# Kernel tuning notes

Hardware: AMD Instinct MI355X
Metric: run time of the kernel (lower is better)

Reference implementation:

```python
import jax, jax.numpy as jnp
import numpy as np
import math

NB_STEPS = 32  # quadrature steps (nb_steps init arg)
HID = 256      # num_hiddens init arg


def _cc_quadrature(nb):
    """Clenshaw-Curtis weights/nodes exactly as in the UMNN reference code."""
    k = np.arange(nb + 1)
    lam = np.cos(np.outer(k, k) * math.pi / nb)
    lam[:, 0] = 0.5
    lam[:, -1] *= 0.5
    lam = lam * 2.0 / nb
    W = k.astype(np.float64).copy()
    W[1::2] = 0.0
    Wv = 2.0 / (1.0 - W ** 2)
    Wv[0] = 1.0
    Wv[1::2] = 0.0
    cc_w = lam.T @ Wv                      # (nb+1,)
    steps = np.cos(k * math.pi / nb)       # (nb+1,) in [-1, 1]
    return cc_w.astype(np.float32), steps.astype(np.float32)

CC_W, CC_STEPS = _cc_quadrature(NB_STEPS)


def setup_inputs() -> dict:
    key = jax.random.key(0)
    ks = jax.random.split(key, 8)
    logits = jax.random.normal(ks[0], (1024, 10), jnp.float32)

    def lin_init(k, shape, fan_in):
        b = 1.0 / np.sqrt(fan_in)
        return jax.random.uniform(k, shape, jnp.float32, -b, b)

    return {
        "logits": logits,
        "W1": lin_init(ks[1], (1, HID), 1),
        "b1": lin_init(ks[2], (HID,), 1),
        "W2": lin_init(ks[3], (HID, HID), HID),
        "b2": lin_init(ks[4], (HID,), HID),
        "W3": lin_init(ks[5], (HID, 1), HID),
        "b3": lin_init(ks[6], (1,), HID),
        "offset": jnp.zeros((1,), jnp.float32),
    }


def _integrand(t, W1, b1, W2, b2, W3, b3):
    # t: (N, S) scalar evaluation points -> strictly positive integrand (N, S)
    h = jax.nn.elu(t[..., None] * W1[0] + b1)                 # (N, S, HID)
    h = jax.nn.elu(jnp.einsum('nsh,hk->nsk', h, W2) + b2)     # (N, S, HID)
    o = jnp.einsum('nsh,ho->nso', h, W3)[..., 0] + b3[0]      # (N, S)
    return jax.nn.elu(o) + 1.0


def reference(logits, W1, b1, W2, b2, W3, b3, offset):
    # 1) log-softmax normalization
    z = logits - jax.nn.logsumexp(logits, axis=1, keepdims=True)
    # 2) standardize with frozen buffers meanlogit=0, logitstd=1 (identity here)
    # 3) flatten and apply monotonic NN: F(x) = offset + int_0^x g(t) dt
    x = z.reshape(-1)                                         # (N,)
    steps = jnp.asarray(CC_STEPS)                             # (S,)
    ccw = jnp.asarray(CC_W)                                   # (S,)
    t = x[:, None] * (steps + 1.0) * 0.5                      # (N, S) nodes in [0, x]
    g = _integrand(t, W1, b1, W2, b2, W3, b3)                 # (N, S)
    integral = (g @ ccw) * (x * 0.5)                          # (N,)
    return (integral + offset[0]).reshape(logits.shape)
```

## Files before the change

kernel.cpp:

```cpp
#include <hip/hip_runtime.h>

typedef _Float16 f16x8 __attribute__((ext_vector_type(8)));
typedef float floatx4 __attribute__((ext_vector_type(4)));

#define NPTS   10240
#define GRID   2112
#define GM1    2111.0f
#define NBLK_MLP 22

#define WS_STEPS 0
#define WS_CCW   256
#define WS_MINX  512
#define WS_X     1024
#define WS_W2IMG 65536
#define WS_G     196608

__device__ __forceinline__ float elu1(float v) {
  return v > 0.f ? v : __expf(v) - 1.f;
}

__device__ __forceinline__ void gload_lds16(const void* g, void* l) {
  __builtin_amdgcn_global_load_lds(
      (const __attribute__((address_space(1))) unsigned int*)g,
      (__attribute__((address_space(3))) unsigned int*)l,
      16, 0, 0);
}

__global__ void k_pre(const float* __restrict__ logits,
                      const float* __restrict__ W2,
                      unsigned char* __restrict__ ws)
{
  __shared__ float red[256];
  const int bid = blockIdx.x, tid = threadIdx.x;
  if (bid < 32) {
    int u    = (bid << 8) + tid;
    int col  = u & 127;
    int rest = u >> 7;
    int k16l = rest & 15;
    int q    = rest >> 4;
    int c    = q >> 1, kh = q & 1;
    int kbase = kh * 128 + k16l * 8;
    int j     = c * 128 + col;
    union { _Float16 h[8]; uint4 v; } pk;
    #pragma unroll
    for (int i = 0; i < 8; ++i)
      pk.h[i] = (_Float16)W2[(kbase + i) * 256 + j];
    unsigned off = (unsigned)q * 32768u + (unsigned)col * 256u
                 + (unsigned)((k16l ^ (col & 7)) << 4);
    *(uint4*)(ws + WS_W2IMG + off) = pk.v;
  } else if (bid == 32) {
    if (tid <= 32) {
      const double pi = 3.141592653589793238462643383279502884;
      float* steps = (float*)(ws + WS_STEPS);
      float* ccw   = (float*)(ws + WS_CCW);
      steps[tid] = (float)cos((double)tid * pi / 32.0);
      double acc = 0.0;
      for (int i = 0; i <= 32; i += 2) {
        double wv = (i == 0) ? 1.0 : 2.0 / (1.0 - (double)(i * i));
        double L  = cos((double)(i * tid) * pi / 32.0);
        if (tid == 0)  L = 0.5;
        if (tid == 32) L *= 0.5;
        acc += L * wv;
      }
      ccw[tid] = (float)(acc * (1.0 / 16.0));
    }
  } else {
    int r = ((bid - 33) << 8) + tid;
    const float* row = logits + r * 10;
    float* x = (float*)(ws + WS_X);
    float v[10]; float m = -3.0e38f;
    #pragma unroll
    for (int c = 0; c < 10; ++c) { v[c] = row[c]; m = fmaxf(m, v[c]); }
    float s = 0.f;
    #pragma unroll
    for (int c = 0; c < 10; ++c) s += __expf(v[c] - m);
    float lse = m + __logf(s);
    float lmin = 3.0e38f;
    #pragma unroll
    for (int c = 0; c < 10; ++c) {
      float z = v[c] - lse;
      x[r * 10 + c] = z;
      lmin = fminf(lmin, z);
    }
    red[tid] = lmin;
    __syncthreads();
    #pragma unroll
    for (int t = 128; t > 0; t >>= 1) {
      if (tid < t) red[tid] = fminf(red[tid], red[tid + t]);
      __syncthreads();
    }
    if (tid == 0)
      atomicMax((unsigned*)(ws + WS_MINX), __float_as_uint(red[0]));
  }
}

__global__ __launch_bounds__(256, 2) void k_mlp(
    const unsigned char* __restrict__ ws,
    const float* __restrict__ W1, const float* __restrict__ b1,
    const float* __restrict__ b2, const float* __restrict__ W3,
    const float* __restrict__ b3)
{
  __shared__ unsigned char smem[65536] __attribute__((aligned(16)));
  const int tid  = threadIdx.x;
  const int lane = tid & 63, wid = tid >> 6;
  const int wm = wid >> 1, wn = wid & 1;
  const int l15 = lane & 15, l4 = lane >> 4;

  const unsigned char* img = ws + WS_W2IMG;
  float* g_out = (float*)(const_cast<unsigned char*>(ws) + WS_G);
  const float minx   = __uint_as_float(*(const unsigned*)(ws + WS_MINX));
  const float step_t = minx * (-1.0f / GM1);

  const int row_base = blockIdx.x * 96;

  #pragma unroll
  for (int i = 0; i < 8; ++i) {
    int off = wid * 1024 + i * 4096;
    gload_lds16(img + off + lane * 16, smem + off);
  }

  float b2r[2][4], w3r[2][4];
  #pragma unroll
  for (int c = 0; c < 2; ++c)
    #pragma unroll
    for (int bj = 0; bj < 4; ++bj) {
      int col = c * 128 + wn * 64 + bj * 16 + l15;
      b2r[c][bj] = b2[col];
      w3r[c][bj] = W3[col];
    }

  f16x8 A[3][8];
  {
    float t[3];
    #pragma unroll
    for (int ai = 0; ai < 3; ++ai) {
      int rg = row_base + wm * 48 + ai * 16 + l15;
      t[ai] = fmaf((float)rg, step_t, minx);
    }
    #pragma unroll
    for (int ks = 0; ks < 8; ++ks) {
      int k0 = ks * 32 + l4 * 8;
      float w1v[8], b1v[8];
      *(float4*)&w1v[0] = *(const float4*)(W1 + k0);
      *(float4*)&w1v[4] = *(const float4*)(W1 + k0 + 4);
      *(float4*)&b1v[0] = *(const float4*)(b1 + k0);
      *(float4*)&b1v[4] = *(const float4*)(b1 + k0 + 4);
      #pragma unroll
      for (int ai = 0; ai < 3; ++ai) {
        union { _Float16 h[8]; f16x8 v; } pk;
        #pragma unroll
        for (int j = 0; j < 8; ++j)
          pk.h[j] = (_Float16)elu1(fmaf(t[ai], w1v[j], b1v[j]));
        A[ai][ks] = pk.v;
      }
    }
  }
  __syncthreads();

  float pacc[3][4];
  #pragma unroll
  for (int a = 0; a < 3; ++a)
    #pragma unroll
    for (int r = 0; r < 4; ++r) pacc[a][r] = 0.f;

  floatx4 acc[3][4];

  #pragma unroll
  for (int q = 0; q < 4; ++q) {
    const int buf = (q & 1) * 32768;
    if (q < 3) {
      const int nb = ((q + 1) & 1) * 32768;
      #pragma unroll
      for (int i = 0; i < 8; ++i) {
        int off = wid * 1024 + i * 4096;
        gload_lds16(img + (q + 1) * 32768 + off + lane * 16, smem + nb + off);
      }
    }
    if ((q & 1) == 0) {
      #pragma unroll
      for (int a = 0; a < 3; ++a)
        #pragma unroll
        for (int bj = 0; bj < 4; ++bj) acc[a][bj] = floatx4{0.f, 0.f, 0.f, 0.f};
    }
    const int kh = q & 1;
    #pragma unroll
    for (int kl = 0; kl < 4; ++kl) {
      const int ks = kh * 4 + kl;
      f16x8 bfr[4];
      #pragma unroll
      for (int bj = 0; bj < 4; ++bj) {
        int col  = wn * 64 + bj * 16 + l15;
        int unit = (kl * 4 + l4) ^ (col & 7);
        bfr[bj]  = *(const f16x8*)(smem + buf + col * 256 + (unit << 4));
      }
      #pragma unroll
      for (int ai = 0; ai < 3; ++ai)
        #pragma unroll
        for (int bj = 0; bj < 4; ++bj)
          acc[ai][bj] = __builtin_amdgcn_mfma_f32_16x16x32_f16(
              A[ai][ks], bfr[bj], acc[ai][bj], 0, 0, 0);
    }
    if (q & 1) {
      const int c = q >> 1;
      #pragma unroll
      for (int bj = 0; bj < 4; ++bj) {
        float b2v = b2r[c][bj], w3v = w3r[c][bj];
        #pragma unroll
        for (int ai = 0; ai < 3; ++ai)
          #pragma unroll
          for (int rr = 0; rr < 4; ++rr)
            pacc[ai][rr] = fmaf(elu1(acc[ai][bj][rr] + b2v), w3v, pacc[ai][rr]);
      }
    }
    __syncthreads();
  }

  float* part = (float*)smem;
  #pragma unroll
  for (int ai = 0; ai < 3; ++ai)
    #pragma unroll
    for (int rr = 0; rr < 4; ++rr) {
      float v = pacc[ai][rr];
      v += __shfl_xor(v, 1);
      v += __shfl_xor(v, 2);
      v += __shfl_xor(v, 4);
      v += __shfl_xor(v, 8);
      if (l15 == 0) part[wid * 48 + ai * 16 + l4 * 4 + rr] = v;
    }
  __syncthreads();
  if (tid < 96) {
    int wmr = tid / 48, r = tid - wmr * 48;
    float o = part[(wmr * 2) * 48 + r] + part[(wmr * 2 + 1) * 48 + r] + b3[0];
    g_out[row_base + wmr * 48 + r] = elu1(o) + 1.f;
  }
}

__global__ void k_interp(const unsigned char* __restrict__ ws,
                         const float* __restrict__ offset,
                         float* __restrict__ out)
{
  __shared__ float gs[GRID];
  __shared__ float st_l[33], cw_l[33];
  const int tid = threadIdx.x;
  const float* gg = (const float*)(ws + WS_G);
  #pragma unroll
  for (int i = tid; i < GRID; i += 256) gs[i] = gg[i];
  if (tid < 33) {
    st_l[tid] = ((const float*)(ws + WS_STEPS))[tid];
    cw_l[tid] = ((const float*)(ws + WS_CCW))[tid];
  }
  __syncthreads();

  const int n = blockIdx.x * 256 + tid;
  const float x    = ((const float*)(ws + WS_X))[n];
  const float minx = __uint_as_float(*(const unsigned*)(ws + WS_MINX));
  const float xo   = x / minx;
  const float a    = xo * (0.5f * GM1);
  const float c0   = GM1 - a;
  float acc = 0.f;
  #pragma unroll 4
  for (int s = 0; s < 33; ++s) {
    float u = fmaf(-a, st_l[s], c0);
    int i = (int)u;
    i = i > (GRID - 2) ? (GRID - 2) : i;
    i = i < 0 ? 0 : i;
    float f  = u - (float)i;
    float g0 = gs[i], g1 = gs[i + 1];
    acc = fmaf(cw_l[s], fmaf(f, g1 - g0, g0), acc);
  }
  out[n] = fmaf(acc, x * 0.5f, offset[0]);
}

extern "C" void kernel_launch(void* const* d_in, const int* in_sizes, int n_in,
                              void* d_out, int out_size, void* d_ws, size_t ws_size,
                              hipStream_t stream)
{
  const float* logits = (const float*)d_in[0];
  const float* W1     = (const float*)d_in[1];
  const float* b1     = (const float*)d_in[2];
  const float* W2     = (const float*)d_in[3];
  const float* b2     = (const float*)d_in[4];
  const float* W3     = (const float*)d_in[5];
  const float* b3     = (const float*)d_in[6];
  const float* offset = (const float*)d_in[7];
  unsigned char* ws   = (unsigned char*)d_ws;
  float* out          = (float*)d_out;

  k_pre<<<37, 256, 0, stream>>>(logits, W2, ws);
  k_mlp<<<NBLK_MLP, 256, 0, stream>>>(ws, W1, b1, b2, W3, b3);
  k_interp<<<40, 256, 0, stream>>>(ws, offset, out);
}
```

Measured before the change: 86.98 us.

## Fuse three kernels into one cooperative kernel with grid-wide syncs

Merges the preprocessing, MLP, and interpolation kernels into a single cooperative launch of 40 blocks, with grid.sync barriers between the phases. The Clenshaw-Curtis nodes and weights are now computed per block in fast float cosine instead of in double precision by a dedicated block. The aim is to remove two kernel launch gaps and the related dependency overhead. The costs are grid-sync latency, a cooperative launch, and slightly lower precision in the quadrature constants.

```diff
diff --git a/kernel.cpp b/kernel.cpp
--- a/kernel.cpp
+++ b/kernel.cpp
@@ -1,15 +1,16 @@
 #include <hip/hip_runtime.h>
+#include <hip/hip_cooperative_groups.h>
+
+namespace cg = cooperative_groups;
 
 typedef _Float16 f16x8 __attribute__((ext_vector_type(8)));
 typedef float floatx4 __attribute__((ext_vector_type(4)));
 
-#define NPTS   10240
-#define GRID   2112
-#define GM1    2111.0f
+#define GRID_T   2112
+#define GM1      2111.0f
 #define NBLK_MLP 22
-
-#define WS_STEPS 0
-#define WS_CCW   256
+#define NBLOCKS  40
+
 #define WS_MINX  512
 #define WS_X     1024
 #define WS_W2IMG 65536
@@ -26,12 +27,18 @@
       16, 0, 0);
 }
 
-__global__ void k_pre(const float* __restrict__ logits,
-                      const float* __restrict__ W2,
-                      unsigned char* __restrict__ ws)
+__global__ __launch_bounds__(256, 2) void k_fused(
+    const float* __restrict__ logits,
+    const float* __restrict__ W1, const float* __restrict__ b1,
+    const float* __restrict__ W2, const float* __restrict__ b2,
+    const float* __restrict__ W3, const float* __restrict__ b3,
+    const float* __restrict__ offset,
+    unsigned char* __restrict__ ws, float* __restrict__ out)
 {
-  __shared__ float red[256];
+  __shared__ unsigned char smem[65536] __attribute__((aligned(16)));
+  cg::grid_group grid = cg::this_grid();
   const int bid = blockIdx.x, tid = threadIdx.x;
+
   if (bid < 32) {
     int u    = (bid << 8) + tid;
     int col  = u & 127;
@@ -48,24 +55,9 @@
     unsigned off = (unsigned)q * 32768u + (unsigned)col * 256u
                  + (unsigned)((k16l ^ (col & 7)) << 4);
     *(uint4*)(ws + WS_W2IMG + off) = pk.v;
-  } else if (bid == 32) {
-    if (tid <= 32) {
-      const double pi = 3.141592653589793238462643383279502884;
-      float* steps = (float*)(ws + WS_STEPS);
-      float* ccw   = (float*)(ws + WS_CCW);
-      steps[tid] = (float)cos((double)tid * pi / 32.0);
-      double acc = 0.0;
-      for (int i = 0; i <= 32; i += 2) {
-        double wv = (i == 0) ? 1.0 : 2.0 / (1.0 - (double)(i * i));
-        double L  = cos((double)(i * tid) * pi / 32.0);
-        if (tid == 0)  L = 0.5;
-        if (tid == 32) L *= 0.5;
-        acc += L * wv;
-      }
-      ccw[tid] = (float)(acc * (1.0 / 16.0));
-    }
-  } else {
-    int r = ((bid - 33) << 8) + tid;
+  } else if (bid < 36) {
+    float* red = (float*)smem;
+    int r = ((bid - 32) << 8) + tid;
     const float* row = logits + r * 10;
     float* x = (float*)(ws + WS_X);
     float v[10]; float m = -3.0e38f;
@@ -92,183 +84,185 @@
     if (tid == 0)
       atomicMax((unsigned*)(ws + WS_MINX), __float_as_uint(red[0]));
   }
-}
-
-__global__ __launch_bounds__(256, 2) void k_mlp(
-    const unsigned char* __restrict__ ws,
-    const float* __restrict__ W1, const float* __restrict__ b1,
-    const float* __restrict__ b2, const float* __restrict__ W3,
-    const float* __restrict__ b3)
-{
-  __shared__ unsigned char smem[65536] __attribute__((aligned(16)));
-  const int tid  = threadIdx.x;
-  const int lane = tid & 63, wid = tid >> 6;
-  const int wm = wid >> 1, wn = wid & 1;
-  const int l15 = lane & 15, l4 = lane >> 4;
-
-  const unsigned char* img = ws + WS_W2IMG;
-  float* g_out = (float*)(const_cast<unsigned char*>(ws) + WS_G);
-  const float minx   = __uint_as_float(*(const unsigned*)(ws + WS_MINX));
-  const float step_t = minx * (-1.0f / GM1);
-
-  const int row_base = blockIdx.x * 96;
-
-  #pragma unroll
-  for (int i = 0; i < 8; ++i) {
-    int off = wid * 1024 + i * 4096;
-    gload_lds16(img + off + lane * 16, smem + off);
+  grid.sync();
+
+  if (bid < NBLK_MLP) {
+    const int lane = tid & 63, wid = tid >> 6;
+    const int wm = wid >> 1, wn = wid & 1;
+    const int l15 = lane & 15, l4 = lane >> 4;
+
+    const unsigned char* img = ws + WS_W2IMG;
+    float* g_out = (float*)(ws + WS_G);
+    const float minx   = __uint_as_float(*(const unsigned*)(ws + WS_MINX));
+    const float step_t = minx * (-1.0f / GM1);
+
+    const int row_base = bid * 96;
+
+    #pragma unroll
+    for (int i = 0; i < 8; ++i) {
+      int off = wid * 1024 + i * 4096;
+      gload_lds16(img + off + lane * 16, smem + off);
+    }
+
+    float b2r[2][4], w3r[2][4];
+    #pragma unroll
+    for (int c = 0; c < 2; ++c)
+      #pragma unroll
+      for (int bj = 0; bj < 4; ++bj) {
+        int col = c * 128 + wn * 64 + bj * 16 + l15;
+        b2r[c][bj] = b2[col];
+        w3r[c][bj] = W3[col];
+      }
+
+    f16x8 A[3][8];
+    {
+      float t[3];
+      #pragma unroll
+      for (int ai = 0; ai < 3; ++ai) {
+        int rg = row_base + wm * 48 + ai * 16 + l15;
+        t[ai] = fmaf((float)rg, step_t, minx);
+      }
+      #pragma unroll
+      for (int ks = 0; ks < 8; ++ks) {
+        int k0 = ks * 32 + l4 * 8;
+        float w1v[8], b1v[8];
+        *(float4*)&w1v[0] = *(const float4*)(W1 + k0);
+        *(float4*)&w1v[4] = *(const float4*)(W1 + k0 + 4);
+        *(float4*)&b1v[0] = *(const float4*)(b1 + k0);
+        *(float4*)&b1v[4] = *(const float4*)(b1 + k0 + 4);
+        #pragma unroll
+        for (int ai = 0; ai < 3; ++ai) {
+          union { _Float16 h[8]; f16x8 v; } pk;
+          #pragma unroll
+          for (int j = 0; j < 8; ++j)
+            pk.h[j] = (_Float16)elu1(fmaf(t[ai], w1v[j], b1v[j]));
+          A[ai][ks] = pk.v;
+        }
+      }
+    }
+    __syncthreads();
+
+    float pacc[3][4];
+    #pragma unroll
+    for (int a = 0; a < 3; ++a)
+      #pragma unroll
+      for (int r = 0; r < 4; ++r) pacc[a][r] = 0.f;
+
+    floatx4 acc[3][4];
+
+    #pragma unroll
+    for (int q = 0; q < 4; ++q) {
+      const int buf = (q & 1) * 32768;
+      if (q < 3) {
+        const int nb = ((q + 1) & 1) * 32768;
+        #pragma unroll
+        for (int i = 0; i < 8; ++i) {
+          int off = wid * 1024 + i * 4096;
+          gload_lds16(img + (q + 1) * 32768 + off + lane * 16, smem + nb + off);
+        }
+      }
+      if ((q & 1) == 0) {
+        #pragma unroll
+        for (int a = 0; a < 3; ++a)
+          #pragma unroll
+          for (int bj = 0; bj < 4; ++bj) acc[a][bj] = floatx4{0.f, 0.f, 0.f, 0.f};
+      }
+      const int kh = q & 1;
+      #pragma unroll
+      for (int kl = 0; kl < 4; ++kl) {
+        const int ks = kh * 4 + kl;
+        f16x8 bfr[4];
+        #pragma unroll
+        for (int bj = 0; bj < 4; ++bj) {
+          int col  = wn * 64 + bj * 16 + l15;
+          int unit = (kl * 4 + l4) ^ (col & 7);
+          bfr[bj]  = *(const f16x8*)(smem + buf + col * 256 + (unit << 4));
+        }
+        #pragma unroll
+        for (int ai = 0; ai < 3; ++ai)
+          #pragma unroll
+          for (int bj = 0; bj < 4; ++bj)
+            acc[ai][bj] = __builtin_amdgcn_mfma_f32_16x16x32_f16(
+                A[ai][ks], bfr[bj], acc[ai][bj], 0, 0, 0);
+      }
+      if (q & 1) {
+        const int c = q >> 1;
+        #pragma unroll
+        for (int bj = 0; bj < 4; ++bj) {
+          float b2v = b2r[c][bj], w3v = w3r[c][bj];
+          #pragma unroll
+          for (int ai = 0; ai < 3; ++ai)
+            #pragma unroll
+            for (int rr = 0; rr < 4; ++rr)
+              pacc[ai][rr] = fmaf(elu1(acc[ai][bj][rr] + b2v), w3v, pacc[ai][rr]);
+        }
+      }
+      __syncthreads();
+    }
+
+    float* part = (float*)smem;
+    #pragma unroll
+    for (int ai = 0; ai < 3; ++ai)
+      #pragma unroll
+      for (int rr = 0; rr < 4; ++rr) {
+        float v = pacc[ai][rr];
+        v += __shfl_xor(v, 1);
+        v += __shfl_xor(v, 2);
+        v += __shfl_xor(v, 4);
+        v += __shfl_xor(v, 8);
+        if (l15 == 0) part[wid * 48 + ai * 16 + l4 * 4 + rr] = v;
+      }
+    __syncthreads();
+    if (tid < 96) {
+      int wmr = tid / 48, r = tid - wmr * 48;
+      float o = part[(wmr * 2) * 48 + r] + part[(wmr * 2 + 1) * 48 + r] + b3[0];
+      g_out[row_base + wmr * 48 + r] = elu1(o) + 1.f;
+    }
   }
-
-  float b2r[2][4], w3r[2][4];
-  #pragma unroll
-  for (int c = 0; c < 2; ++c)
-    #pragma unroll
-    for (int bj = 0; bj < 4; ++bj) {
-      int col = c * 128 + wn * 64 + bj * 16 + l15;
-      b2r[c][bj] = b2[col];
-      w3r[c][bj] = W3[col];
-    }
-
-  f16x8 A[3][8];
+  grid.sync();
+
   {
-    float t[3];
-    #pragma unroll
-    for (int ai = 0; ai < 3; ++ai) {
-      int rg = row_base + wm * 48 + ai * 16 + l15;
-      t[ai] = fmaf((float)rg, step_t, minx);
-    }
-    #pragma unroll
-    for (int ks = 0; ks < 8; ++ks) {
-      int k0 = ks * 32 + l4 * 8;
-      float w1v[8], b1v[8];
-      *(float4*)&w1v[0] = *(const float4*)(W1 + k0);
-      *(float4*)&w1v[4] = *(const float4*)(W1 + k0 + 4);
-      *(float4*)&b1v[0] = *(const float4*)(b1 + k0);
-      *(float4*)&b1v[4] = *(const float4*)(b1 + k0 + 4);
-      #pragma unroll
-      for (int ai = 0; ai < 3; ++ai) {
-        union { _Float16 h[8]; f16x8 v; } pk;
-        #pragma unroll
-        for (int j = 0; j < 8; ++j)
-          pk.h[j] = (_Float16)elu1(fmaf(t[ai], w1v[j], b1v[j]));
-        A[ai][ks] = pk.v;
-      }
-    }
+    float* gs   = (float*)smem;
+    float* st_l = (float*)(smem + GRID_T * 4);
+    float* cw_l = st_l + 33;
+    if (tid <= 32) {
+      const float pi32 = 3.14159265358979323846f / 32.f;
+      st_l[tid] = __cosf((float)tid * pi32);
+      float acc = 0.f;
+      #pragma unroll
+      for (int i = 0; i <= 32; i += 2) {
+        float wv = (i == 0) ? 1.f : 2.f / (1.f - (float)(i * i));
+        float L  = __cosf((float)((i * tid) & 63) * pi32);
+        if (tid == 0)  L = 0.5f;
+        if (tid == 32) L *= 0.5f;
+        acc += L * wv;
+      }
+      cw_l[tid] = acc * (1.0f / 16.0f);
+    }
+    const float* gg = (const float*)(ws + WS_G);
+    #pragma unroll
+    for (int i = tid; i < GRID_T; i += 256) gs[i] = gg[i];
+    __syncthreads();
+
+    const int n = bid * 256 + tid;
+    const float x    = ((const float*)(ws + WS_X))[n];
+    const float minx = __uint_as_float(*(const unsigned*)(ws + WS_MINX));
+    const float xo   = x / minx;
+    const float a    = xo * (0.5f * GM1);
+    const float c0   = GM1 - a;
+    float acc = 0.f;
+    #pragma unroll 4
+    for (int s = 0; s < 33; ++s) {
+      float u = fmaf(-a, st_l[s], c0);
+      int i = (int)u;
+      i = i > (GRID_T - 2) ? (GRID_T - 2) : i;
+      i = i < 0 ? 0 : i;
+      float f  = u - (float)i;
+      float g0 = gs[i], g1 = gs[i + 1];
+      acc = fmaf(cw_l[s], fmaf(f, g1 - g0, g0), acc);
+    }
+    out[n] = fmaf(acc, x * 0.5f, offset[0]);
   }
-  __syncthreads();
-
-  float pacc[3][4];
-  #pragma unroll
-  for (int a = 0; a < 3; ++a)
-    #pragma unroll
-    for (int r = 0; r < 4; ++r) pacc[a][r] = 0.f;
-
-  floatx4 acc[3][4];
-
-  #pragma unroll
-  for (int q = 0; q < 4; ++q) {
-    const int buf = (q & 1) * 32768;
-    if (q < 3) {
-      const int nb = ((q + 1) & 1) * 32768;
-      #pragma unroll
-      for (int i = 0; i < 8; ++i) {
-        int off = wid * 1024 + i * 4096;
-        gload_lds16(img + (q + 1) * 32768 + off + lane * 16, smem + nb + off);
-      }
-    }
-    if ((q & 1) == 0) {
-      #pragma unroll
-      for (int a = 0; a < 3; ++a)
-        #pragma unroll
-        for (int bj = 0; bj < 4; ++bj) acc[a][bj] = floatx4{0.f, 0.f, 0.f, 0.f};
-    }
-    const int kh = q & 1;
-    #pragma unroll
-    for (int kl = 0; kl < 4; ++kl) {
-      const int ks = kh * 4 + kl;
-      f16x8 bfr[4];
-      #pragma unroll
-      for (int bj = 0; bj < 4; ++bj) {
-        int col  = wn * 64 + bj * 16 + l15;
-        int unit = (kl * 4 + l4) ^ (col & 7);
-        bfr[bj]  = *(const f16x8*)(smem + buf + col * 256 + (unit << 4));
-      }
-      #pragma unroll
-      for (int ai = 0; ai < 3; ++ai)
-        #pragma unroll
-        for (int bj = 0; bj < 4; ++bj)
-          acc[ai][bj] = __builtin_amdgcn_mfma_f32_16x16x32_f16(
-              A[ai][ks], bfr[bj], acc[ai][bj], 0, 0, 0);
-    }
-    if (q & 1) {
-      const int c = q >> 1;
-      #pragma unroll
-      for (int bj = 0; bj < 4; ++bj) {
-        float b2v = b2r[c][bj], w3v = w3r[c][bj];
-        #pragma unroll
-        for (int ai = 0; ai < 3; ++ai)
-          #pragma unroll
-          for (int rr = 0; rr < 4; ++rr)
-            pacc[ai][rr] = fmaf(elu1(acc[ai][bj][rr] + b2v), w3v, pacc[ai][rr]);
-      }
-    }
-    __syncthreads();
-  }
-
-  float* part = (float*)smem;
-  #pragma unroll
-  for (int ai = 0; ai < 3; ++ai)
-    #pragma unroll
-    for (int rr = 0; rr < 4; ++rr) {
-      float v = pacc[ai][rr];
-      v += __shfl_xor(v, 1);
-      v += __shfl_xor(v, 2);
-      v += __shfl_xor(v, 4);
-      v += __shfl_xor(v, 8);
-      if (l15 == 0) part[wid * 48 + ai * 16 + l4 * 4 + rr] = v;
-    }
-  __syncthreads();
-  if (tid < 96) {
-    int wmr = tid / 48, r = tid - wmr * 48;
-    float o = part[(wmr * 2) * 48 + r] + part[(wmr * 2 + 1) * 48 + r] + b3[0];
-    g_out[row_base + wmr * 48 + r] = elu1(o) + 1.f;
-  }
-}
-
-__global__ void k_interp(const unsigned char* __restrict__ ws,
-                         const float* __restrict__ offset,
-                         float* __restrict__ out)
-{
-  __shared__ float gs[GRID];
-  __shared__ float st_l[33], cw_l[33];
-  const int tid = threadIdx.x;
-  const float* gg = (const float*)(ws + WS_G);
-  #pragma unroll
-  for (int i = tid; i < GRID; i += 256) gs[i] = gg[i];
-  if (tid < 33) {
-    st_l[tid] = ((const float*)(ws + WS_STEPS))[tid];
-    cw_l[tid] = ((const float*)(ws + WS_CCW))[tid];
-  }
-  __syncthreads();
-
-  const int n = blockIdx.x * 256 + tid;
-  const float x    = ((const float*)(ws + WS_X))[n];
-  const float minx = __uint_as_float(*(const unsigned*)(ws + WS_MINX));
-  const float xo   = x / minx;
-  const float a    = xo * (0.5f * GM1);
-  const float c0   = GM1 - a;
-  float acc = 0.f;
-  #pragma unroll 4
-  for (int s = 0; s < 33; ++s) {
-    float u = fmaf(-a, st_l[s], c0);
-    int i = (int)u;
-    i = i > (GRID - 2) ? (GRID - 2) : i;
-    i = i < 0 ? 0 : i;
-    float f  = u - (float)i;
-    float g0 = gs[i], g1 = gs[i + 1];
-    acc = fmaf(cw_l[s], fmaf(f, g1 - g0, g0), acc);
-  }
-  out[n] = fmaf(acc, x * 0.5f, offset[0]);
 }
 
 extern "C" void kernel_launch(void* const* d_in, const int* in_sizes, int n_in,
@@ -284,9 +278,11 @@
   const float* b3     = (const float*)d_in[6];
   const float* offset = (const float*)d_in[7];
   unsigned char* ws   = (unsigned char*)d_ws;
-  float* out          = (float*)d_out;
-
-  k_pre<<<37, 256, 0, stream>>>(logits, W2, ws);
-  k_mlp<<<NBLK_MLP, 256, 0, stream>>>(ws, W1, b1, b2, W3, b3);
-  k_interp<<<40, 256, 0, stream>>>(ws, offset, out);
-}
+  float* outp         = (float*)d_out;
+
+  void* args[] = {(void*)&logits, (void*)&W1, (void*)&b1, (void*)&W2,
+                  (void*)&b2, (void*)&W3, (void*)&b3, (void*)&offset,
+                  (void*)&ws, (void*)&outp};
+  hipLaunchCooperativeKernel((void*)k_fused, dim3(NBLOCKS), dim3(256),
+                             args, 0, stream);
+}
```

Result: slower. 120.5 us (+38.6%).
